# Optimization experiments

Hardware: AMD Instinct MI355X
Metric: run time of the kernel (lower is better)

Reference implementation:

```python
import jax, jax.numpy as jnp
import numpy as np

HIDDEN = 1024
MOE_FF = 512
SHARED_FF = 2816
NUM_EXPERTS = 16
TOP_K = 2
NORM_TOPK = True


def setup_inputs() -> dict:
    key = jax.random.key(0)
    ks = jax.random.split(key, 8)
    s = 0.02
    return {
        "layer_input": jax.random.normal(ks[0], (1, 2048, HIDDEN), dtype=jnp.float32),
        "gate_w": jax.random.normal(ks[1], (NUM_EXPERTS, HIDDEN), dtype=jnp.float32) * s,
        # fused gate_up weight per expert, laid out for x @ W: [E, hidden, 2*moe_ff]
        "w_gate_up": jax.random.normal(ks[2], (NUM_EXPERTS, HIDDEN, 2 * MOE_FF), dtype=jnp.float32) * s,
        # down weight per expert, laid out for h @ W: [E, moe_ff, hidden]
        "w_down": jax.random.normal(ks[3], (NUM_EXPERTS, MOE_FF, HIDDEN), dtype=jnp.float32) * s,
        # shared expert (Qwen2MoeMLP): Linear weights stored torch-style [out, in]
        "shared_w_gate": jax.random.normal(ks[4], (SHARED_FF, HIDDEN), dtype=jnp.float32) * s,
        "shared_w_up": jax.random.normal(ks[5], (SHARED_FF, HIDDEN), dtype=jnp.float32) * s,
        "shared_w_down": jax.random.normal(ks[6], (HIDDEN, SHARED_FF), dtype=jnp.float32) * s,
        "shared_gate_w": jax.random.normal(ks[7], (1, HIDDEN), dtype=jnp.float32) * s,
    }


def reference(layer_input, gate_w, w_gate_up, w_down,
              shared_w_gate, shared_w_up, shared_w_down, shared_gate_w):
    B, S, D = layer_input.shape
    x = layer_input.reshape(-1, D)  # [N, D]
    N = x.shape[0]

    # shared expert: silu-gated MLP, scaled by per-token sigmoid gate
    shared = (jax.nn.silu(x @ shared_w_gate.T) * (x @ shared_w_up.T)) @ shared_w_down.T
    shared = shared * jax.nn.sigmoid(x @ shared_gate_w.T)  # [N, D]

    # router: softmax in float32, top-k, optional renorm
    logits = x @ gate_w.T  # [N, E]
    probs = jax.nn.softmax(logits.astype(jnp.float32), axis=-1)
    rw, sel = jax.lax.top_k(probs, TOP_K)  # [N, K]
    if NORM_TOPK:
        rw = rw / rw.sum(axis=-1, keepdims=True)
    rw = rw.astype(x.dtype)

    # dense combine weights: zero for unselected experts (equivalent to
    # the sort/dispatch + grouped-GEMM + weighted scatter-combine)
    combine = jnp.zeros((N, NUM_EXPERTS), x.dtype).at[jnp.arange(N)[:, None], sel].set(rw)

    # expert gate_up projection, SwiGLU, down projection, weighted combine
    gu = jnp.einsum('nd,edf->nef', x, w_gate_up)  # [N, E, 2*moe_ff]
    g, h = jnp.split(gu, 2, axis=-1)
    h = jax.nn.silu(g) * h  # [N, E, moe_ff]
    expert_out = jnp.einsum('nef,efd,ne->nd', h, w_down, combine)  # [N, D]

    out = expert_out + shared
    return out.reshape(B, S, D)
```

## Files before the change

kernel.cpp:

```cpp
#include <hip/hip_runtime.h>
#include <hip/hip_bf16.h>

typedef unsigned short ushort_t;
typedef __bf16 bf16x8 __attribute__((ext_vector_type(8)));
typedef float f32x4 __attribute__((ext_vector_type(4)));

#define N_TOK 2048
#define DH    1024
#define FF    512
#define SFF   2816
#define NE    16

#define GBM 64
#define DBM 64
#define BN 64
#define BK 64
#define LDK 72

__device__ __forceinline__ ushort_t f2bf(float f) {
  unsigned int x = __float_as_uint(f);
  unsigned int lsb = (x >> 16) & 1u;
  x += 0x7fffu + lsb;
  return (ushort_t)(x >> 16);
}
__device__ __forceinline__ float bf2f(ushort_t u) {
  union { unsigned int i; float f; } v; v.i = ((unsigned int)u) << 16; return v.f;
}
__device__ __forceinline__ unsigned int cvtpk(float lo, float hi) {
  unsigned int r;
  asm("v_cvt_pk_bf16_f32 %0, %1, %2" : "=v"(r) : "v"(lo), "v"(hi));
  return r;
}
__device__ __forceinline__ uint4 cvt8v(const float4 a, const float4 b) {
  uint4 v;
  v.x = cvtpk(a.x, a.y); v.y = cvtpk(a.z, a.w);
  v.z = cvtpk(b.x, b.y); v.w = cvtpk(b.z, b.w);
  return v;
}
__device__ __forceinline__ uint4 ld_cvt8(const float* __restrict__ p) {
  float4 a = *(const float4*)p;
  float4 b = *(const float4*)(p + 4);
  return cvt8v(a, b);
}

__global__ void router_kernel(const float* __restrict__ X, const float* __restrict__ GW,
                              const float* __restrict__ SGW,
                              int* __restrict__ sel, float* __restrict__ wtk,
                              float* __restrict__ sgate) {
  int wave = threadIdx.x >> 6, lane = threadIdx.x & 63;
  int n = blockIdx.x * 4 + wave;
  const float* x = X + (size_t)n * DH;
  int e = lane & 15, s = lane >> 4;
  const float* gw = GW + (size_t)e * DH;
  float lg = 0.f;
  #pragma unroll
  for (int i = 0; i < 64; ++i) {
    int d = s * 256 + i * 4;
    float4 xv = *(const float4*)(x + d);
    float4 gv = *(const float4*)(gw + d);
    lg += xv.x * gv.x + xv.y * gv.y + xv.z * gv.z + xv.w * gv.w;
  }
  lg += __shfl_down(lg, 32);
  lg += __shfl_down(lg, 16);

  float gd = 0.f;
  #pragma unroll
  for (int i = 0; i < 4; ++i) {
    int d = lane * 16 + i * 4;
    float4 xv = *(const float4*)(x + d);
    float4 gv = *(const float4*)(SGW + d);
    gd += xv.x * gv.x + xv.y * gv.y + xv.z * gv.z + xv.w * gv.w;
  }
  #pragma unroll
  for (int off = 32; off >= 1; off >>= 1) gd += __shfl_down(gd, off);

  float l[16];
  #pragma unroll
  for (int i = 0; i < 16; ++i) l[i] = __shfl(lg, i);

  if (lane == 0) {
    int i1 = 0; float v1 = l[0];
    #pragma unroll
    for (int i = 1; i < 16; ++i) if (l[i] > v1) { v1 = l[i]; i1 = i; }
    int i2 = -1; float v2 = -1e30f;
    #pragma unroll
    for (int i = 0; i < 16; ++i) { if (i == i1) continue; if (l[i] > v2) { v2 = l[i]; i2 = i; } }
    float p2 = __expf(v2 - v1);
    float inv = 1.f / (1.f + p2);
    sel[n * 2 + 0] = i1; sel[n * 2 + 1] = i2;
    wtk[n * 2 + 0] = inv; wtk[n * 2 + 1] = p2 * inv;
    sgate[n] = 1.f / (1.f + __expf(-gd));
  }
}

__global__ void scatter_kernel(const int* __restrict__ sel,
                               int* __restrict__ toks, int* __restrict__ slot_of,
                               int* __restrict__ offs) {
  __shared__ int cnt[NE], bas[NE];
  int t = threadIdx.x;
  if (t < NE) cnt[t] = 0;
  __syncthreads();
  for (int i = t; i < N_TOK * 2; i += 256) atomicAdd(&cnt[sel[i]], 1);
  __syncthreads();
  if (t == 0) {
    int s = 0;
    for (int e = 0; e < NE; ++e) { bas[e] = s; offs[e] = s; s += cnt[e]; }
    offs[NE] = s;
  }
  __syncthreads();
  if (t < NE) cnt[t] = 0;
  __syncthreads();
  for (int i = t; i < N_TOK * 2; i += 256) {
    int e = sel[i];
    int p = atomicAdd(&cnt[e], 1);
    int slot = bas[e] + p;
    toks[slot] = i >> 1;
    slot_of[i] = slot;
  }
}

__global__ __launch_bounds__(256, 4) void gateup_kernel(
    const float* __restrict__ X, const float* __restrict__ WGU,
    const float* __restrict__ SWG, const float* __restrict__ SWU,
    ushort_t* __restrict__ HX, ushort_t* __restrict__ HS,
    const int* __restrict__ toks, const int* __restrict__ offs) {
  __shared__ __align__(16) ushort_t As[GBM][LDK];
  __shared__ __align__(16) ushort_t Bgs[BN][LDK];
  __shared__ __align__(16) ushort_t Bus[BN][LDK];
  const int K = DH, NT = K / BK;

  int bid = blockIdx.x;
  int t = threadIdx.x;
  int wave = t >> 6, lane = t & 63;
  int wm = wave & 1, wn = wave >> 1;
  int qd = lane >> 4, l16 = lane & 15;
  int sr = t >> 3, sc = (t & 7) * 8;

  f32x4 accg[2][2], accu[2][2];
  #pragma unroll
  for (int i = 0; i < 2; ++i)
    #pragma unroll
    for (int j = 0; j < 2; ++j) {
      accg[i][j] = (f32x4){0.f, 0.f, 0.f, 0.f};
      accu[i][j] = (f32x4){0.f, 0.f, 0.f, 0.f};
    }

  int m0, n0, M, base, is_exp;

  if (bid < 1408) {
    is_exp = 0; base = 0; M = N_TOK;
    n0 = (bid % 44) * BN; m0 = (bid / 44) * GBM;
    const float* arow[2];
    const float *bgrow[2], *burow[2];
    #pragma unroll
    for (int p = 0; p < 2; ++p)
      arow[p] = X + (size_t)(m0 + sr + 32 * p) * K + sc;
    #pragma unroll
    for (int p = 0; p < 2; ++p) {
      bgrow[p] = SWG + (size_t)(n0 + sr + 32 * p) * K + sc;
      burow[p] = SWU + (size_t)(n0 + sr + 32 * p) * K + sc;
    }
    uint4 ar[2], bgr[2], bur[2];
    #pragma unroll
    for (int p = 0; p < 2; ++p) { ar[p] = ld_cvt8(arow[p]); bgr[p] = ld_cvt8(bgrow[p]); bur[p] = ld_cvt8(burow[p]); }

    for (int kt = 0; kt < NT; ++kt) {
      #pragma unroll
      for (int p = 0; p < 2; ++p) {
        *(uint4*)&As[sr + 32 * p][sc] = ar[p];
        *(uint4*)&Bgs[sr + 32 * p][sc] = bgr[p];
        *(uint4*)&Bus[sr + 32 * p][sc] = bur[p];
      }
      __syncthreads();
      if (kt + 1 < NT) {
        int ko = (kt + 1) * BK;
        #pragma unroll
        for (int p = 0; p < 2; ++p) { ar[p] = ld_cvt8(arow[p] + ko); bgr[p] = ld_cvt8(bgrow[p] + ko); bur[p] = ld_cvt8(burow[p] + ko); }
      }
      #pragma unroll
      for (int ks = 0; ks < 2; ++ks) {
        int kk = ks * 32 + qd * 8;
        bf16x8 af[2], bgf[2], buf[2];
        #pragma unroll
        for (int i = 0; i < 2; ++i)
          af[i] = *(const bf16x8*)&As[wm * 32 + i * 16 + l16][kk];
        #pragma unroll
        for (int j = 0; j < 2; ++j) {
          bgf[j] = *(const bf16x8*)&Bgs[wn * 32 + j * 16 + l16][kk];
          buf[j] = *(const bf16x8*)&Bus[wn * 32 + j * 16 + l16][kk];
        }
        #pragma unroll
        for (int i = 0; i < 2; ++i)
          #pragma unroll
          for (int j = 0; j < 2; ++j) {
            accg[i][j] = __builtin_amdgcn_mfma_f32_16x16x32_bf16(af[i], bgf[j], accg[i][j], 0, 0, 0);
            accu[i][j] = __builtin_amdgcn_mfma_f32_16x16x32_bf16(af[i], buf[j], accu[i][j], 0, 0, 0);
          }
      }
      __syncthreads();
    }
  } else {
    is_exp = 1;
    int b2 = bid - 1408;
    int e = b2 >> 8, rem = b2 & 255;
    n0 = (rem & 7) * BN; m0 = (rem >> 3) * GBM;
    base = offs[e]; M = offs[e + 1] - base;
    if (m0 >= M) return;
    const float* W = WGU + (size_t)e * DH * (2 * FF);
    int tn = t & 63, tk = (t >> 6) * 16;

    const float* arow[2];
    #pragma unroll
    for (int p = 0; p < 2; ++p) {
      int m = m0 + sr + 32 * p;
      int mm = m < M ? m : (M - 1);
      arow[p] = X + (size_t)toks[base + mm] * K + sc;
    }
    const float* wkb = W + (size_t)tk * (2 * FF) + n0 + tn;

    uint4 ar[2];
    float bgr[16], bur[16];
    #pragma unroll
    for (int p = 0; p < 2; ++p) ar[p] = ld_cvt8(arow[p]);
    #pragma unroll
    for (int j = 0; j < 16; ++j) {
      bgr[j] = wkb[(size_t)j * (2 * FF)];
      bur[j] = wkb[(size_t)j * (2 * FF) + FF];
    }

    for (int kt = 0; kt < NT; ++kt) {
      #pragma unroll
      for (int p = 0; p < 2; ++p)
        *(uint4*)&As[sr + 32 * p][sc] = ar[p];
      {
        uint4 g0, g1, u0, u1;
        g0.x = cvtpk(bgr[0], bgr[1]);  g0.y = cvtpk(bgr[2], bgr[3]);
        g0.z = cvtpk(bgr[4], bgr[5]);  g0.w = cvtpk(bgr[6], bgr[7]);
        g1.x = cvtpk(bgr[8], bgr[9]);  g1.y = cvtpk(bgr[10], bgr[11]);
        g1.z = cvtpk(bgr[12], bgr[13]); g1.w = cvtpk(bgr[14], bgr[15]);
        u0.x = cvtpk(bur[0], bur[1]);  u0.y = cvtpk(bur[2], bur[3]);
        u0.z = cvtpk(bur[4], bur[5]);  u0.w = cvtpk(bur[6], bur[7]);
        u1.x = cvtpk(bur[8], bur[9]);  u1.y = cvtpk(bur[10], bur[11]);
        u1.z = cvtpk(bur[12], bur[13]); u1.w = cvtpk(bur[14], bur[15]);
        *(uint4*)&Bgs[tn][tk]     = g0;
        *(uint4*)&Bgs[tn][tk + 8] = g1;
        *(uint4*)&Bus[tn][tk]     = u0;
        *(uint4*)&Bus[tn][tk + 8] = u1;
      }
      __syncthreads();
      if (kt + 1 < NT) {
        int ko = (kt + 1) * BK;
        #pragma unroll
        for (int p = 0; p < 2; ++p) ar[p] = ld_cvt8(arow[p] + ko);
        const float* wk = wkb + (size_t)ko * (2 * FF);
        #pragma unroll
        for (int j = 0; j < 16; ++j) {
          bgr[j] = wk[(size_t)j * (2 * FF)];
          bur[j] = wk[(size_t)j * (2 * FF) + FF];
        }
      }
      #pragma unroll
      for (int ks = 0; ks < 2; ++ks) {
        int kk = ks * 32 + qd * 8;
        bf16x8 af[2], bgf[2], buf[2];
        #pragma unroll
        for (int i = 0; i < 2; ++i)
          af[i] = *(const bf16x8*)&As[wm * 32 + i * 16 + l16][kk];
        #pragma unroll
        for (int j = 0; j < 2; ++j) {
          bgf[j] = *(const bf16x8*)&Bgs[wn * 32 + j * 16 + l16][kk];
          buf[j] = *(const bf16x8*)&Bus[wn * 32 + j * 16 + l16][kk];
        }
        #pragma unroll
        for (int i = 0; i < 2; ++i)
          #pragma unroll
          for (int j = 0; j < 2; ++j) {
            accg[i][j] = __builtin_amdgcn_mfma_f32_16x16x32_bf16(af[i], bgf[j], accg[i][j], 0, 0, 0);
            accu[i][j] = __builtin_amdgcn_mfma_f32_16x16x32_bf16(af[i], buf[j], accu[i][j], 0, 0, 0);
          }
      }
      __syncthreads();
    }
  }

  #pragma unroll
  for (int i = 0; i < 2; ++i)
    #pragma unroll
    for (int r = 0; r < 4; ++r) {
      int row = wm * 32 + i * 16 + qd * 4 + r;
      #pragma unroll
      for (int j = 0; j < 2; ++j) {
        float g = accg[i][j][r], u = accu[i][j][r];
        float h = g / (1.f + __expf(-g)) * u;
        As[row][wn * 32 + j * 16 + l16] = f2bf(h);
      }
    }
  __syncthreads();
  if (is_exp) {
    #pragma unroll
    for (int p = 0; p < 2; ++p) {
      int m = m0 + sr + 32 * p;
      if (m < M)
        *(uint4*)(HX + (size_t)(base + m) * FF + n0 + sc) = *(uint4*)&As[sr + 32 * p][sc];
    }
  } else {
    #pragma unroll
    for (int p = 0; p < 2; ++p) {
      int m = m0 + sr + 32 * p;
      *(uint4*)(HS + (size_t)m * SFF + n0 + sc) = *(uint4*)&As[sr + 32 * p][sc];
    }
  }
}

__global__ __launch_bounds__(256, 4) void down_kernel(
    const ushort_t* __restrict__ HX, const ushort_t* __restrict__ HS,
    const float* __restrict__ WDN, const float* __restrict__ SWD,
    ushort_t* __restrict__ SD0, ushort_t* __restrict__ SD1,
    ushort_t* __restrict__ EXPO, const int* __restrict__ offs) {
  __shared__ __align__(16) ushort_t As[DBM][LDK];
  __shared__ __align__(16) ushort_t Bs[BN][LDK];

  int bid = blockIdx.x;
  int t = threadIdx.x;
  int wave = t >> 6, lane = t & 63;
  int wm = wave & 1, wn = wave >> 1;
  int qd = lane >> 4, l16 = lane & 15;
  int sr = t >> 3, sc = (t & 7) * 8;

  f32x4 c[2][2];
  #pragma unroll
  for (int i = 0; i < 2; ++i)
    #pragma unroll
    for (int j = 0; j < 2; ++j) c[i][j] = (f32x4){0.f, 0.f, 0.f, 0.f};

  int m0, n0, M, base_row;
  ushort_t* outp;

  if (bid < 1024) {
    int kz = bid >> 9, rem = bid & 511;
    m0 = (rem >> 4) * DBM; n0 = (rem & 15) * BN;
    M = N_TOK; base_row = 0;
    const int KC = SFF / 2, NT = KC / BK;
    int kb = kz * KC;
    outp = kz ? SD1 : SD0;

    const ushort_t* arow[2];
    const float* brow[2];
    #pragma unroll
    for (int p = 0; p < 2; ++p) {
      arow[p] = HS + (size_t)(m0 + sr + 32 * p) * SFF + kb + sc;
      brow[p] = SWD + (size_t)(n0 + sr + 32 * p) * SFF + kb + sc;
    }

    uint4 ar[2], br[2];
    #pragma unroll
    for (int p = 0; p < 2; ++p) { ar[p] = *(const uint4*)(arow[p]); br[p] = ld_cvt8(brow[p]); }

    for (int kt = 0; kt < NT; ++kt) {
      #pragma unroll
      for (int p = 0; p < 2; ++p) {
        *(uint4*)&As[sr + 32 * p][sc] = ar[p];
        *(uint4*)&Bs[sr + 32 * p][sc] = br[p];
      }
      __syncthreads();
      if (kt + 1 < NT) {
        int ko = (kt + 1) * BK;
        #pragma unroll
        for (int p = 0; p < 2; ++p) { ar[p] = *(const uint4*)(arow[p] + ko); br[p] = ld_cvt8(brow[p] + ko); }
      }
      #pragma unroll
      for (int ks = 0; ks < 2; ++ks) {
        int kk = ks * 32 + qd * 8;
        bf16x8 af[2], bf[2];
        #pragma unroll
        for (int i = 0; i < 2; ++i)
          af[i] = *(const bf16x8*)&As[wm * 32 + i * 16 + l16][kk];
        #pragma unroll
        for (int j = 0; j < 2; ++j)
          bf[j] = *(const bf16x8*)&Bs[wn * 32 + j * 16 + l16][kk];
        #pragma unroll
        for (int i = 0; i < 2; ++i)
          #pragma unroll
          for (int j = 0; j < 2; ++j)
            c[i][j] = __builtin_amdgcn_mfma_f32_16x16x32_bf16(af[i], bf[j], c[i][j], 0, 0, 0);
      }
      __syncthreads();
    }
  } else {
    int b2 = bid - 1024;
    int e = b2 >> 9, rem = b2 & 511;
    m0 = (rem >> 4) * DBM; n0 = (rem & 15) * BN;
    int base = offs[e];
    M = offs[e + 1] - base;
    if (m0 >= M) return;
    base_row = base;
    const int NT = FF / BK;
    const float* W = WDN + (size_t)e * FF * DH;
    const ushort_t* A = HX + (size_t)base * FF;
    int tn = t & 63, tk = (t >> 6) * 16;
    outp = EXPO;

    const ushort_t* arow[2];
    #pragma unroll
    for (int p = 0; p < 2; ++p) {
      int m = m0 + sr + 32 * p;
      int mm = m < M ? m : (M - 1);
      arow[p] = A + (size_t)mm * FF + sc;
    }
    const float* wkb = W + (size_t)tk * DH + n0 + tn;

    uint4 ar[2];
    float br[16];
    #pragma unroll
    for (int p = 0; p < 2; ++p) ar[p] = *(const uint4*)(arow[p]);
    #pragma unroll
    for (int j = 0; j < 16; ++j) br[j] = wkb[(size_t)j * DH];

    for (int kt = 0; kt < NT; ++kt) {
      #pragma unroll
      for (int p = 0; p < 2; ++p)
        *(uint4*)&As[sr + 32 * p][sc] = ar[p];
      {
        uint4 b0, b1;
        b0.x = cvtpk(br[0], br[1]);   b0.y = cvtpk(br[2], br[3]);
        b0.z = cvtpk(br[4], br[5]);   b0.w = cvtpk(br[6], br[7]);
        b1.x = cvtpk(br[8], br[9]);   b1.y = cvtpk(br[10], br[11]);
        b1.z = cvtpk(br[12], br[13]); b1.w = cvtpk(br[14], br[15]);
        *(uint4*)&Bs[tn][tk]     = b0;
        *(uint4*)&Bs[tn][tk + 8] = b1;
      }
      __syncthreads();
      if (kt + 1 < NT) {
        int ko = (kt + 1) * BK;
        #pragma unroll
        for (int p = 0; p < 2; ++p) ar[p] = *(const uint4*)(arow[p] + ko);
        const float* wk = wkb + (size_t)ko * DH;
        #pragma unroll
        for (int j = 0; j < 16; ++j) br[j] = wk[(size_t)j * DH];
      }
      #pragma unroll
      for (int ks = 0; ks < 2; ++ks) {
        int kk = ks * 32 + qd * 8;
        bf16x8 af[2], bf[2];
        #pragma unroll
        for (int i = 0; i < 2; ++i)
          af[i] = *(const bf16x8*)&As[wm * 32 + i * 16 + l16][kk];
        #pragma unroll
        for (int j = 0; j < 2; ++j)
          bf[j] = *(const bf16x8*)&Bs[wn * 32 + j * 16 + l16][kk];
        #pragma unroll
        for (int i = 0; i < 2; ++i)
          #pragma unroll
          for (int j = 0; j < 2; ++j)
            c[i][j] = __builtin_amdgcn_mfma_f32_16x16x32_bf16(af[i], bf[j], c[i][j], 0, 0, 0);
      }
      __syncthreads();
    }
  }

  #pragma unroll
  for (int i = 0; i < 2; ++i)
    #pragma unroll
    for (int r = 0; r < 4; ++r) {
      int row = wm * 32 + i * 16 + qd * 4 + r;
      #pragma unroll
      for (int j = 0; j < 2; ++j)
        As[row][wn * 32 + j * 16 + l16] = f2bf(c[i][j][r]);
    }
  __syncthreads();
  #pragma unroll
  for (int p = 0; p < 2; ++p) {
    int m = m0 + sr + 32 * p;
    if (m < M)
      *(uint4*)(outp + (size_t)(base_row + m) * DH + n0 + sc) = *(uint4*)&As[sr + 32 * p][sc];
  }
}

__global__ void combine_kernel(const ushort_t* __restrict__ SD0, const ushort_t* __restrict__ SD1,
                               const ushort_t* __restrict__ EXPO,
                               const float* __restrict__ sgate, const float* __restrict__ wtk,
                               const int* __restrict__ slot_of, float* __restrict__ out) {
  int n = blockIdx.x, t = threadIdx.x;
  float sg = sgate[n];
  float w0 = wtk[n * 2 + 0], w1 = wtk[n * 2 + 1];
  int s0 = slot_of[n * 2 + 0], s1 = slot_of[n * 2 + 1];
  int col = t * 4;
  ushort4 d0 = *(const ushort4*)(SD0 + (size_t)n * DH + col);
  ushort4 d1 = *(const ushort4*)(SD1 + (size_t)n * DH + col);
  ushort4 a  = *(const ushort4*)(EXPO + (size_t)s0 * DH + col);
  ushort4 b  = *(const ushort4*)(EXPO + (size_t)s1 * DH + col);
  float4 o;
  o.x = sg * (bf2f(d0.x) + bf2f(d1.x)) + w0 * bf2f(a.x) + w1 * bf2f(b.x);
  o.y = sg * (bf2f(d0.y) + bf2f(d1.y)) + w0 * bf2f(a.y) + w1 * bf2f(b.y);
  o.z = sg * (bf2f(d0.z) + bf2f(d1.z)) + w0 * bf2f(a.z) + w1 * bf2f(b.z);
  o.w = sg * (bf2f(d0.w) + bf2f(d1.w)) + w0 * bf2f(a.w) + w1 * bf2f(b.w);
  *(float4*)(out + (size_t)n * DH + col) = o;
}

extern "C" void kernel_launch(void* const* d_in, const int* in_sizes, int n_in,
                              void* d_out, int out_size, void* d_ws, size_t ws_size,
                              hipStream_t stream) {
  const float* x    = (const float*)d_in[0];
  const float* gw   = (const float*)d_in[1];
  const float* wgu  = (const float*)d_in[2];
  const float* wdn  = (const float*)d_in[3];
  const float* swg  = (const float*)d_in[4];
  const float* swu  = (const float*)d_in[5];
  const float* swd  = (const float*)d_in[6];
  const float* sgw  = (const float*)d_in[7];
  float* out = (float*)d_out;

  char* ws = (char*)d_ws;
  constexpr size_t OFF_HS   = 0;
  constexpr size_t OFF_HX   = OFF_HS   + (size_t)N_TOK * SFF * 2;
  constexpr size_t OFF_SD0  = OFF_HX   + (size_t)4096 * FF * 2;
  constexpr size_t OFF_SD1  = OFF_SD0  + (size_t)N_TOK * DH * 2;
  constexpr size_t OFF_EXPO = OFF_SD1  + (size_t)N_TOK * DH * 2;
  constexpr size_t OFF_TOK  = OFF_EXPO + (size_t)4096 * DH * 2;
  constexpr size_t OFF_OFFS = OFF_TOK  + 4096 * 4;
  constexpr size_t OFF_SEL  = OFF_OFFS + 32 * 4;
  constexpr size_t OFF_WTK  = OFF_SEL  + 4096 * 4;
  constexpr size_t OFF_SG   = OFF_WTK  + 4096 * 4;
  constexpr size_t OFF_SLOT = OFF_SG   + 2048 * 4;

  ushort_t* hs    = (ushort_t*)(ws + OFF_HS);
  ushort_t* hx    = (ushort_t*)(ws + OFF_HX);
  ushort_t* sd0   = (ushort_t*)(ws + OFF_SD0);
  ushort_t* sd1   = (ushort_t*)(ws + OFF_SD1);
  ushort_t* expo  = (ushort_t*)(ws + OFF_EXPO);
  int*      toks  = (int*)(ws + OFF_TOK);
  int*      offs  = (int*)(ws + OFF_OFFS);
  int*      sel   = (int*)(ws + OFF_SEL);
  float*    wtk   = (float*)(ws + OFF_WTK);
  float*    sgate = (float*)(ws + OFF_SG);
  int*      slot_of = (int*)(ws + OFF_SLOT);

  router_kernel<<<N_TOK / 4, 256, 0, stream>>>(x, gw, sgw, sel, wtk, sgate);
  scatter_kernel<<<1, 256, 0, stream>>>(sel, toks, slot_of, offs);
  gateup_kernel<<<1408 + 4096, 256, 0, stream>>>(x, wgu, swg, swu, hx, hs, toks, offs);
  down_kernel<<<1024 + 8192, 256, 0, stream>>>(hx, hs, wdn, swd, sd0, sd1, expo, offs);
  combine_kernel<<<N_TOK, 256, 0, stream>>>(sd0, sd1, expo, sgate, wtk, slot_of, out);
}
```

Baseline: 377.3 us.

## Fuse token scatter into router via global atomics, drop shared down split-K

The single-block scatter kernel is removed. The router now appends each token into fixed-capacity per-expert slots with global atomics, so expert GEMMs read a count instead of prefix offsets. The shared-expert down projection no longer splits K into two halves, which removes one partial output buffer and its extra read in combine. In exchange, token order inside an expert becomes nondeterministic, the slot clamp at CAP can silently overwrite tokens if an expert receives more than 1024, and the shared down GEMM runs with half as many blocks, each doing twice the K work.

```diff
diff --git a/kernel.cpp b/kernel.cpp
--- a/kernel.cpp
+++ b/kernel.cpp
@@ -10,6 +10,7 @@
 #define FF    512
 #define SFF   2816
 #define NE    16
+#define CAP   1024
 
 #define GBM 64
 #define DBM 64
@@ -45,8 +46,9 @@
 
 __global__ void router_kernel(const float* __restrict__ X, const float* __restrict__ GW,
                               const float* __restrict__ SGW,
-                              int* __restrict__ sel, float* __restrict__ wtk,
-                              float* __restrict__ sgate) {
+                              int* __restrict__ toks, int* __restrict__ slot_of,
+                              float* __restrict__ wtk, float* __restrict__ sgate,
+                              int* __restrict__ cnt) {
   int wave = threadIdx.x >> 6, lane = threadIdx.x & 63;
   int n = blockIdx.x * 4 + wave;
   const float* x = X + (size_t)n * DH;
@@ -87,35 +89,13 @@
     for (int i = 0; i < 16; ++i) { if (i == i1) continue; if (l[i] > v2) { v2 = l[i]; i2 = i; } }
     float p2 = __expf(v2 - v1);
     float inv = 1.f / (1.f + p2);
-    sel[n * 2 + 0] = i1; sel[n * 2 + 1] = i2;
+    int p0 = atomicAdd(&cnt[i1], 1); if (p0 >= CAP) p0 = CAP - 1;
+    int p1 = atomicAdd(&cnt[i2], 1); if (p1 >= CAP) p1 = CAP - 1;
+    int s0 = i1 * CAP + p0, s1 = i2 * CAP + p1;
+    toks[s0] = n; toks[s1] = n;
+    slot_of[n * 2 + 0] = s0; slot_of[n * 2 + 1] = s1;
     wtk[n * 2 + 0] = inv; wtk[n * 2 + 1] = p2 * inv;
     sgate[n] = 1.f / (1.f + __expf(-gd));
-  }
-}
-
-__global__ void scatter_kernel(const int* __restrict__ sel,
-                               int* __restrict__ toks, int* __restrict__ slot_of,
-                               int* __restrict__ offs) {
-  __shared__ int cnt[NE], bas[NE];
-  int t = threadIdx.x;
-  if (t < NE) cnt[t] = 0;
-  __syncthreads();
-  for (int i = t; i < N_TOK * 2; i += 256) atomicAdd(&cnt[sel[i]], 1);
-  __syncthreads();
-  if (t == 0) {
-    int s = 0;
-    for (int e = 0; e < NE; ++e) { bas[e] = s; offs[e] = s; s += cnt[e]; }
-    offs[NE] = s;
-  }
-  __syncthreads();
-  if (t < NE) cnt[t] = 0;
-  __syncthreads();
-  for (int i = t; i < N_TOK * 2; i += 256) {
-    int e = sel[i];
-    int p = atomicAdd(&cnt[e], 1);
-    int slot = bas[e] + p;
-    toks[slot] = i >> 1;
-    slot_of[i] = slot;
   }
 }
 
@@ -123,7 +103,7 @@
     const float* __restrict__ X, const float* __restrict__ WGU,
     const float* __restrict__ SWG, const float* __restrict__ SWU,
     ushort_t* __restrict__ HX, ushort_t* __restrict__ HS,
-    const int* __restrict__ toks, const int* __restrict__ offs) {
+    const int* __restrict__ toks, const int* __restrict__ CNT) {
   __shared__ __align__(16) ushort_t As[GBM][LDK];
   __shared__ __align__(16) ushort_t Bgs[BN][LDK];
   __shared__ __align__(16) ushort_t Bus[BN][LDK];
@@ -204,7 +184,7 @@
     int b2 = bid - 1408;
     int e = b2 >> 8, rem = b2 & 255;
     n0 = (rem & 7) * BN; m0 = (rem >> 3) * GBM;
-    base = offs[e]; M = offs[e + 1] - base;
+    base = e * CAP; M = CNT[e];
     if (m0 >= M) return;
     const float* W = WGU + (size_t)e * DH * (2 * FF);
     int tn = t & 63, tk = (t >> 6) * 16;
@@ -315,8 +295,8 @@
 __global__ __launch_bounds__(256, 4) void down_kernel(
     const ushort_t* __restrict__ HX, const ushort_t* __restrict__ HS,
     const float* __restrict__ WDN, const float* __restrict__ SWD,
-    ushort_t* __restrict__ SD0, ushort_t* __restrict__ SD1,
-    ushort_t* __restrict__ EXPO, const int* __restrict__ offs) {
+    ushort_t* __restrict__ SD, ushort_t* __restrict__ EXPO,
+    const int* __restrict__ CNT) {
   __shared__ __align__(16) ushort_t As[DBM][LDK];
   __shared__ __align__(16) ushort_t Bs[BN][LDK];
 
@@ -336,20 +316,18 @@
   int m0, n0, M, base_row;
   ushort_t* outp;
 
-  if (bid < 1024) {
-    int kz = bid >> 9, rem = bid & 511;
-    m0 = (rem >> 4) * DBM; n0 = (rem & 15) * BN;
+  if (bid < 512) {
+    m0 = (bid >> 4) * DBM; n0 = (bid & 15) * BN;
     M = N_TOK; base_row = 0;
-    const int KC = SFF / 2, NT = KC / BK;
-    int kb = kz * KC;
-    outp = kz ? SD1 : SD0;
+    const int NT = SFF / BK;
+    outp = SD;
 
     const ushort_t* arow[2];
     const float* brow[2];
     #pragma unroll
     for (int p = 0; p < 2; ++p) {
-      arow[p] = HS + (size_t)(m0 + sr + 32 * p) * SFF + kb + sc;
-      brow[p] = SWD + (size_t)(n0 + sr + 32 * p) * SFF + kb + sc;
+      arow[p] = HS + (size_t)(m0 + sr + 32 * p) * SFF + sc;
+      brow[p] = SWD + (size_t)(n0 + sr + 32 * p) * SFF + sc;
     }
 
     uint4 ar[2], br[2];
@@ -387,11 +365,11 @@
       __syncthreads();
     }
   } else {
-    int b2 = bid - 1024;
+    int b2 = bid - 512;
     int e = b2 >> 9, rem = b2 & 511;
     m0 = (rem >> 4) * DBM; n0 = (rem & 15) * BN;
-    int base = offs[e];
-    M = offs[e + 1] - base;
+    int base = e * CAP;
+    M = CNT[e];
     if (m0 >= M) return;
     base_row = base;
     const int NT = FF / BK;
@@ -476,7 +454,7 @@
   }
 }
 
-__global__ void combine_kernel(const ushort_t* __restrict__ SD0, const ushort_t* __restrict__ SD1,
+__global__ void combine_kernel(const ushort_t* __restrict__ SD,
                                const ushort_t* __restrict__ EXPO,
                                const float* __restrict__ sgate, const float* __restrict__ wtk,
                                const int* __restrict__ slot_of, float* __restrict__ out) {
@@ -485,15 +463,14 @@
   float w0 = wtk[n * 2 + 0], w1 = wtk[n * 2 + 1];
   int s0 = slot_of[n * 2 + 0], s1 = slot_of[n * 2 + 1];
   int col = t * 4;
-  ushort4 d0 = *(const ushort4*)(SD0 + (size_t)n * DH + col);
-  ushort4 d1 = *(const ushort4*)(SD1 + (size_t)n * DH + col);
+  ushort4 d0 = *(const ushort4*)(SD + (size_t)n * DH + col);
   ushort4 a  = *(const ushort4*)(EXPO + (size_t)s0 * DH + col);
   ushort4 b  = *(const ushort4*)(EXPO + (size_t)s1 * DH + col);
   float4 o;
-  o.x = sg * (bf2f(d0.x) + bf2f(d1.x)) + w0 * bf2f(a.x) + w1 * bf2f(b.x);
-  o.y = sg * (bf2f(d0.y) + bf2f(d1.y)) + w0 * bf2f(a.y) + w1 * bf2f(b.y);
-  o.z = sg * (bf2f(d0.z) + bf2f(d1.z)) + w0 * bf2f(a.z) + w1 * bf2f(b.z);
-  o.w = sg * (bf2f(d0.w) + bf2f(d1.w)) + w0 * bf2f(a.w) + w1 * bf2f(b.w);
+  o.x = sg * bf2f(d0.x) + w0 * bf2f(a.x) + w1 * bf2f(b.x);
+  o.y = sg * bf2f(d0.y) + w0 * bf2f(a.y) + w1 * bf2f(b.y);
+  o.z = sg * bf2f(d0.z) + w0 * bf2f(a.z) + w1 * bf2f(b.z);
+  o.w = sg * bf2f(d0.w) + w0 * bf2f(a.w) + w1 * bf2f(b.w);
   *(float4*)(out + (size_t)n * DH + col) = o;
 }
 
@@ -513,31 +490,27 @@
   char* ws = (char*)d_ws;
   constexpr size_t OFF_HS   = 0;
   constexpr size_t OFF_HX   = OFF_HS   + (size_t)N_TOK * SFF * 2;
-  constexpr size_t OFF_SD0  = OFF_HX   + (size_t)4096 * FF * 2;
-  constexpr size_t OFF_SD1  = OFF_SD0  + (size_t)N_TOK * DH * 2;
-  constexpr size_t OFF_EXPO = OFF_SD1  + (size_t)N_TOK * DH * 2;
-  constexpr size_t OFF_TOK  = OFF_EXPO + (size_t)4096 * DH * 2;
-  constexpr size_t OFF_OFFS = OFF_TOK  + 4096 * 4;
-  constexpr size_t OFF_SEL  = OFF_OFFS + 32 * 4;
-  constexpr size_t OFF_WTK  = OFF_SEL  + 4096 * 4;
+  constexpr size_t OFF_SD   = OFF_HX   + (size_t)NE * CAP * FF * 2;
+  constexpr size_t OFF_EXPO = OFF_SD   + (size_t)N_TOK * DH * 2;
+  constexpr size_t OFF_TOK  = OFF_EXPO + (size_t)NE * CAP * DH * 2;
+  constexpr size_t OFF_SLOT = OFF_TOK  + (size_t)NE * CAP * 4;
+  constexpr size_t OFF_WTK  = OFF_SLOT + 4096 * 4;
   constexpr size_t OFF_SG   = OFF_WTK  + 4096 * 4;
-  constexpr size_t OFF_SLOT = OFF_SG   + 2048 * 4;
+  constexpr size_t OFF_CNT  = OFF_SG   + 2048 * 4;
 
   ushort_t* hs    = (ushort_t*)(ws + OFF_HS);
   ushort_t* hx    = (ushort_t*)(ws + OFF_HX);
-  ushort_t* sd0   = (ushort_t*)(ws + OFF_SD0);
-  ushort_t* sd1   = (ushort_t*)(ws + OFF_SD1);
+  ushort_t* sd    = (ushort_t*)(ws + OFF_SD);
   ushort_t* expo  = (ushort_t*)(ws + OFF_EXPO);
   int*      toks  = (int*)(ws + OFF_TOK);
-  int*      offs  = (int*)(ws + OFF_OFFS);
-  int*      sel   = (int*)(ws + OFF_SEL);
+  int*      slot_of = (int*)(ws + OFF_SLOT);
   float*    wtk   = (float*)(ws + OFF_WTK);
   float*    sgate = (float*)(ws + OFF_SG);
-  int*      slot_of = (int*)(ws + OFF_SLOT);
-
-  router_kernel<<<N_TOK / 4, 256, 0, stream>>>(x, gw, sgw, sel, wtk, sgate);
-  scatter_kernel<<<1, 256, 0, stream>>>(sel, toks, slot_of, offs);
-  gateup_kernel<<<1408 + 4096, 256, 0, stream>>>(x, wgu, swg, swu, hx, hs, toks, offs);
-  down_kernel<<<1024 + 8192, 256, 0, stream>>>(hx, hs, wdn, swd, sd0, sd1, expo, offs);
-  combine_kernel<<<N_TOK, 256, 0, stream>>>(sd0, sd1, expo, sgate, wtk, slot_of, out);
-}
+  int*      cnt   = (int*)(ws + OFF_CNT);
+
+  hipMemsetAsync(cnt, 0, NE * sizeof(int), stream);
+  router_kernel<<<N_TOK / 4, 256, 0, stream>>>(x, gw, sgw, toks, slot_of, wtk, sgate, cnt);
+  gateup_kernel<<<1408 + 4096, 256, 0, stream>>>(x, wgu, swg, swu, hx, hs, toks, cnt);
+  down_kernel<<<512 + 8192, 256, 0, stream>>>(hx, hs, wdn, swd, sd, expo, cnt);
+  combine_kernel<<<N_TOK, 256, 0, stream>>>(sd, expo, sgate, wtk, slot_of, out);
+}
```

After: 419.9 us. 11.3% more time.
